# Optimization experiments

Measured on AMD Instinct MI355X. Metric: run time of the kernel, lower is better.

The kernel has to match this reference:

```python
import jax, jax.numpy as jnp
import numpy as np

B, N, M, C = 2, 8192, 8192, 3
SRC_W = 1.0  # src_weight * loss_src_weight
DST_W = 1.0  # dst_weight * loss_dst_weight


def setup_inputs() -> dict:
    key = jax.random.key(0)
    k1, k2 = jax.random.split(key)
    source = jax.random.normal(k1, (B, N, C), dtype=jnp.float32)
    target = jax.random.normal(k2, (B, M, C), dtype=jnp.float32)
    return {"source": source, "target": target}


def reference(source, target):
    # mode='l2' -> mse_loss(none) summed over C = squared euclidean distance
    # distance: [B, N, M]
    diff = source[:, :, None, :] - target[:, None, :, :]  # [B,N,M,C]
    distance = jnp.sum(diff * diff, axis=-1)
    src2dst = jnp.min(distance, axis=2)       # [B,N]
    indices1 = jnp.argmin(distance, axis=2)   # [B,N]
    dst2src = jnp.min(distance, axis=1)       # [B,M]
    indices2 = jnp.argmin(distance, axis=1)   # [B,M]
    # reduction='mean', weights all 1.0
    loss_src = jnp.mean(src2dst * SRC_W)
    loss_dst = jnp.mean(dst2src * DST_W)
    return (loss_src, loss_dst, indices1, indices2)
```

## Files before the change

### kernel.cpp

```cpp
#include <hip/hip_runtime.h>
#include <math.h>


static constexpr int Bn = 2;
static constexpr int Nn = 8192;
static constexpr int THR = 256;
static constexpr int QPL = 4;
static constexpr int RT = 1024;
static constexpr int WROWS = 256;
static constexpr int CT = 64;
static constexpr int TB = 8;
static constexpr int CB = 4096;

typedef __attribute__((ext_vector_type(2))) float f32x2;

__device__ __forceinline__ f32x2 pk_add(f32x2 a, f32x2 b) {
    f32x2 r;
    asm("v_pk_add_f32 %0, %1, %2" : "=v"(r) : "v"(a), "v"(b));
    return r;
}
__device__ __forceinline__ f32x2 pk_mul(f32x2 a, f32x2 b) {
    f32x2 r;
    asm("v_pk_mul_f32 %0, %1, %2" : "=v"(r) : "v"(a), "v"(b));
    return r;
}
__device__ __forceinline__ f32x2 fmin2(f32x2 a, f32x2 b) {
    f32x2 r;
    r.x = fminf(a.x, b.x);
    r.y = fminf(a.y, b.y);
    return r;
}
__device__ __forceinline__ f32x2 dist3x2(f32x2 tx, f32x2 ty, f32x2 tz,
                                         f32x2 nqx, f32x2 nqy, f32x2 nqz) {
    f32x2 dx = pk_add(tx, nqx);
    f32x2 dy = pk_add(ty, nqy);
    f32x2 dz = pk_add(tz, nqz);
    f32x2 px = pk_mul(dx, dx);
    f32x2 py = pk_mul(dy, dy);
    f32x2 pz = pk_mul(dz, dz);
    return pk_add(pk_add(px, py), pz);
}

template <int PAT>
__device__ __forceinline__ float swzx(float x) {
    return __int_as_float(__builtin_amdgcn_ds_swizzle(__float_as_int(x), PAT));
}
static constexpr int SWZ_X1  = 0x041F;
static constexpr int SWZ_X2  = 0x081F;
static constexpr int SWZ_X4  = 0x101F;
static constexpr int SWZ_X8  = 0x201F;
static constexpr int SWZ_X16 = 0x401F;

__device__ __forceinline__ float dist3(float s0, float s1, float s2,
                                       float q0, float q1, float q2) {
    #pragma clang fp contract(off)
    float d0 = s0 - q0;
    float d1 = s1 - q1;
    float d2 = s2 - q2;
    return (d0 * d0 + d1 * d1) + d2 * d2;
}

__global__ void cd_init(unsigned long long* __restrict__ ws) {
    int i = blockIdx.x * blockDim.x + threadIdx.x;
    if (i < 2 * Bn * Nn) ws[i] = 0xFFFFFFFFFFFFFFFFULL;
}

__global__ __launch_bounds__(THR, 4) void cd_tile(const float* __restrict__ S,
                                                  const float* __restrict__ T,
                                                  unsigned long long* __restrict__ ws) {
    const int b = blockIdx.z;
    const int rbase = blockIdx.x * RT;
    const int cbase = blockIdx.y * CT;
    unsigned long long* wsRow = ws + (size_t)b * Nn;
    unsigned long long* wsCol = ws + 2 * Nn + (size_t)b * Nn;

    __shared__ alignas(16) float lt[3][CT];
    __shared__ unsigned long long lwcol[4][CT];
    if (threadIdx.x < CT * 3 / 4) {
        float4 v4 = ((const float4*)(T + ((size_t)b * Nn + cbase) * 3))[threadIdx.x];
        int e = threadIdx.x * 4;
        lt[(e    ) % 3][(e    ) / 3] = v4.x;
        lt[(e + 1) % 3][(e + 1) / 3] = v4.y;
        lt[(e + 2) % 3][(e + 2) / 3] = v4.z;
        lt[(e + 3) % 3][(e + 3) / 3] = v4.w;
    }
    __syncthreads();

    const int w = threadIdx.x >> 6;
    const int L = threadIdx.x & 63;
    const int rowA = rbase + w * WROWS + L;
    const unsigned int anchor = (unsigned int)(rbase + w * WROWS);

    f32x2 nqx[QPL], nqy[QPL], nqz[QPL];
    #pragma unroll
    for (int k = 0; k < QPL; ++k) {
        const float* p = S + ((size_t)b * Nn + rowA + k * 64) * 3;
        float a0 = -p[0], a1 = -p[1], a2 = -p[2];
        nqx[k].x = a0; nqx[k].y = a0;
        nqy[k].x = a1; nqy[k].y = a1;
        nqz[k].x = a2; nqz[k].y = a2;
    }

    float best[QPL];
    int bb[QPL];
    #pragma unroll
    for (int k = 0; k < QPL; ++k) { best[k] = INFINITY; bb[k] = 0; }

    #pragma unroll 2
    for (int jb = 0; jb < CT / TB; ++jb) {
        const f32x2* lx = (const f32x2*)&lt[0][jb * TB];
        const f32x2* ly = (const f32x2*)&lt[1][jb * TB];
        const f32x2* lz = (const f32x2*)&lt[2][jb * TB];
        f32x2 tx[4], ty[4], tz[4];
        #pragma unroll
        for (int p = 0; p < 4; ++p) { tx[p] = lx[p]; ty[p] = ly[p]; tz[p] = lz[p]; }

        f32x2 cm2[4];
        #pragma unroll
        for (int k = 0; k < QPL; ++k) {
            f32x2 dd[4];
            #pragma unroll
            for (int p = 0; p < 4; ++p)
                dd[p] = dist3x2(tx[p], ty[p], tz[p], nqx[k], nqy[k], nqz[k]);
            #pragma unroll
            for (int p = 0; p < 4; ++p)
                cm2[p] = (k == 0) ? dd[p] : fmin2(cm2[p], dd[p]);
            float m0 = fminf(fminf(dd[0].x, dd[0].y), dd[1].x);
            float m1 = fminf(fminf(dd[1].y, dd[2].x), dd[2].y);
            float m2 = fminf(dd[3].x, dd[3].y);
            float bmin = fminf(fminf(m0, m1), m2);
            if (bmin < best[k]) { best[k] = bmin; bb[k] = cbase + jb * TB; }
        }

        float cmf0 = cm2[0].x, cmf1 = cm2[0].y, cmf2 = cm2[1].x, cmf3 = cm2[1].y;
        float cmf4 = cm2[2].x, cmf5 = cm2[2].y, cmf6 = cm2[3].x, cmf7 = cm2[3].y;

        const bool u1 = (L & 1);
        float a0 = fminf(u1 ? cmf4 : cmf0, swzx<SWZ_X1>(u1 ? cmf0 : cmf4));
        float a1 = fminf(u1 ? cmf5 : cmf1, swzx<SWZ_X1>(u1 ? cmf1 : cmf5));
        float a2 = fminf(u1 ? cmf6 : cmf2, swzx<SWZ_X1>(u1 ? cmf2 : cmf6));
        float a3 = fminf(u1 ? cmf7 : cmf3, swzx<SWZ_X1>(u1 ? cmf3 : cmf7));
        const bool u2 = (L & 2);
        float b0 = fminf(u2 ? a2 : a0, swzx<SWZ_X2>(u2 ? a0 : a2));
        float b1 = fminf(u2 ? a3 : a1, swzx<SWZ_X2>(u2 ? a1 : a3));
        const bool u4 = (L & 4);
        float c0 = fminf(u4 ? b1 : b0, swzx<SWZ_X4>(u4 ? b0 : b1));
        c0 = fminf(c0, swzx<SWZ_X8>(c0));
        c0 = fminf(c0, swzx<SWZ_X16>(c0));
        c0 = fminf(c0, __shfl_xor(c0, 32, 64));

        if (L < TB) {
            const int c = 4 * (L & 1) + 2 * ((L >> 1) & 1) + ((L >> 2) & 1);
            unsigned long long pk =
                ((unsigned long long)__float_as_uint(c0) << 32) | anchor;
            lwcol[w][jb * TB + c] = pk;
        }
    }

    #pragma unroll
    for (int k = 0; k < QPL; ++k) {
        unsigned long long pk =
            ((unsigned long long)__float_as_uint(best[k]) << 32) |
            (unsigned int)bb[k];
        atomicMin(&wsRow[rowA + k * 64], pk);
    }

    __syncthreads();
    if (threadIdx.x < CT) {
        unsigned long long x0 = lwcol[0][threadIdx.x];
        unsigned long long x1 = lwcol[1][threadIdx.x];
        unsigned long long x2 = lwcol[2][threadIdx.x];
        unsigned long long x3 = lwcol[3][threadIdx.x];
        unsigned long long m01 = x0 < x1 ? x0 : x1;
        unsigned long long m23 = x2 < x3 ? x2 : x3;
        unsigned long long m = m01 < m23 ? m01 : m23;
        atomicMin(&wsCol[cbase + threadIdx.x], m);
    }
}

__global__ __launch_bounds__(256) void cd_fin(const unsigned long long* __restrict__ ws,
                                              const float* __restrict__ S,
                                              const float* __restrict__ T,
                                              float* __restrict__ out,
                                              float* __restrict__ pr,
                                              float* __restrict__ pc) {
    __shared__ float red[4];
    const int tid = threadIdx.x;

    if (blockIdx.x < CB) {
        const int e = blockIdx.x * 4 + (tid >> 6);
        const int L = tid & 63;
        const int b = e >> 13;
        const int col = e & 8191;

        unsigned long long p = ws[2 * Nn + e];
        const float m = __uint_as_float((unsigned int)(p >> 32));
        const int A = (int)(unsigned int)(p & 0xFFFFFFFFu);

        const float* tc = T + ((size_t)b * Nn + col) * 3;
        const float t0 = tc[0], t1 = tc[1], t2 = tc[2];

        const float4* Sp = (const float4*)(S + ((size_t)b * Nn + A + L * 4) * 3);
        const float4 x0 = Sp[0], x1 = Sp[1], x2 = Sp[2];

        int found = 0x7FFFFFFF;
        if (dist3(x2.y, x2.z, x2.w, t0, t1, t2) == m) found = A + L * 4 + 3;
        if (dist3(x1.z, x1.w, x2.x, t0, t1, t2) == m) found = A + L * 4 + 2;
        if (dist3(x0.w, x1.x, x1.y, t0, t1, t2) == m) found = A + L * 4 + 1;
        if (dist3(x0.x, x0.y, x0.z, t0, t1, t2) == m) found = A + L * 4 + 0;
        #pragma unroll
        for (int mask = 1; mask < 64; mask <<= 1)
            found = min(found, __shfl_xor(found, mask, 64));
        if (L == 0) out[2 + 2 * Nn + e] = (float)found;

        if (L == 0) red[tid >> 6] = m;
        __syncthreads();
        if (tid == 0) pc[blockIdx.x] = (red[0] + red[1]) + (red[2] + red[3]);
    } else {
        const int j = (blockIdx.x - CB) * 256 + tid;
        const int b = j >> 13;
        const int row = j & 8191;

        unsigned long long p = ws[j];
        const float dist = __uint_as_float((unsigned int)(p >> 32));
        const int cb = (int)(unsigned int)(p & 0xFFFFFFFFu);

        const float* Pp = S + ((size_t)b * Nn + row) * 3;
        const float s0 = Pp[0], s1 = Pp[1], s2 = Pp[2];
        const float4* Qb = (const float4*)(T + ((size_t)b * Nn + cb) * 3);
        const float4 y0 = Qb[0], y1 = Qb[1], y2 = Qb[2];
        const float4 y3 = Qb[3], y4 = Qb[4], y5 = Qb[5];

        int idx = cb;
        if (dist3(s0, s1, s2, y5.y, y5.z, y5.w) == dist) idx = cb + 7;
        if (dist3(s0, s1, s2, y4.z, y4.w, y5.x) == dist) idx = cb + 6;
        if (dist3(s0, s1, s2, y3.w, y4.x, y4.y) == dist) idx = cb + 5;
        if (dist3(s0, s1, s2, y3.x, y3.y, y3.z) == dist) idx = cb + 4;
        if (dist3(s0, s1, s2, y2.y, y2.z, y2.w) == dist) idx = cb + 3;
        if (dist3(s0, s1, s2, y1.z, y1.w, y2.x) == dist) idx = cb + 2;
        if (dist3(s0, s1, s2, y0.w, y1.x, y1.y) == dist) idx = cb + 1;
        if (dist3(s0, s1, s2, y0.x, y0.y, y0.z) == dist) idx = cb + 0;
        out[2 + j] = (float)idx;

        float sum = dist;
        for (int off = 32; off > 0; off >>= 1) sum += __shfl_down(sum, off, 64);
        if ((tid & 63) == 0) red[tid >> 6] = sum;
        __syncthreads();
        if (tid == 0)
            pr[blockIdx.x - CB] = (red[0] + red[1]) + (red[2] + red[3]);
    }
}

__global__ __launch_bounds__(256) void cd_combine(const float* __restrict__ pr,
                                                  const float* __restrict__ pc,
                                                  float* __restrict__ out) {
    const int tid = threadIdx.x;
    float s1 = (tid < 64) ? pr[tid] : 0.0f;
    float s2 = 0.0f;
    for (int i = tid; i < CB; i += 256) s2 += pc[i];

    __shared__ float r1[4], r2[4];
    for (int off = 32; off > 0; off >>= 1) {
        s1 += __shfl_down(s1, off, 64);
        s2 += __shfl_down(s2, off, 64);
    }
    if ((tid & 63) == 0) { r1[tid >> 6] = s1; r2[tid >> 6] = s2; }
    __syncthreads();
    if (tid == 0) {
        out[0] = ((r1[0] + r1[1]) + (r1[2] + r1[3])) / (float)(Bn * Nn);
        out[1] = ((r2[0] + r2[1]) + (r2[2] + r2[3])) / (float)(Bn * Nn);
    }
}

static constexpr int FPTS = 256;
static constexpr int FCHUNK = 1024;

__global__ void cd_zero2(float* __restrict__ out) { out[0] = 0.0f; out[1] = 0.0f; }

__global__ __launch_bounds__(FPTS) void cd_dir_direct(const float* __restrict__ P,
                                                      const float* __restrict__ Q,
                                                      int nP, int nQ,
                                                      float* __restrict__ idx_out,
                                                      float* __restrict__ loss_out,
                                                      float inv_count) {
    __shared__ float lq[FCHUNK * 3];
    __shared__ float red[FPTS / 64];
    const int b = blockIdx.z;
    const int i = blockIdx.x * FPTS + threadIdx.x;
    const float* Pp = P + ((size_t)b * nP + i) * 3;
    const float s0 = Pp[0], s1 = Pp[1], s2 = Pp[2];

    float best = INFINITY;
    int bi = 0;
    for (int c = 0; c < nQ / FCHUNK; ++c) {
        __syncthreads();
        const float* Qb = Q + ((size_t)b * nQ + (size_t)c * FCHUNK) * 3;
        for (int j = threadIdx.x; j < FCHUNK * 3; j += FPTS) lq[j] = Qb[j];
        __syncthreads();
        #pragma unroll 4
        for (int m = 0; m < FCHUNK; ++m) {
            float dist = dist3(s0, s1, s2, lq[3 * m], lq[3 * m + 1], lq[3 * m + 2]);
            if (dist < best) { best = dist; bi = c * FCHUNK + m; }
        }
    }
    idx_out[(size_t)b * nP + i] = (float)bi;

    float v = best;
    for (int off = 32; off > 0; off >>= 1) v += __shfl_down(v, off, 64);
    const int wid = threadIdx.x >> 6;
    if ((threadIdx.x & 63) == 0) red[wid] = v;
    __syncthreads();
    if (threadIdx.x == 0) {
        float a = 0.0f;
        for (int w = 0; w < FPTS / 64; ++w) a += red[w];
        atomicAdd(loss_out, a * inv_count);
    }
}

extern "C" void kernel_launch(void* const* d_in, const int* in_sizes, int n_in,
                              void* d_out, int out_size, void* d_ws, size_t ws_size,
                              hipStream_t stream) {
    const float* src = (const float*)d_in[0];
    const float* tgt = (const float*)d_in[1];
    float* out = (float*)d_out;
    const int TOTAL = 2 * Bn * Nn;
    const size_t need = (size_t)TOTAL * sizeof(unsigned long long)
                      + (64 + CB) * sizeof(float);

    if (ws_size >= need) {
        unsigned long long* ws = (unsigned long long*)d_ws;
        float* pr = (float*)(ws + TOTAL);
        float* pc = pr + 64;
        cd_init<<<(TOTAL + 255) / 256, 256, 0, stream>>>(ws);
        cd_tile<<<dim3(Nn / RT, Nn / CT, Bn), THR, 0, stream>>>(src, tgt, ws);
        cd_fin<<<CB + 64, 256, 0, stream>>>(ws, src, tgt, out, pr, pc);
        cd_combine<<<1, 256, 0, stream>>>(pr, pc, out);
    } else {
        cd_zero2<<<1, 1, 0, stream>>>(out);
        cd_dir_direct<<<dim3(Nn / FPTS, 1, Bn), FPTS, 0, stream>>>(
            src, tgt, Nn, Nn, out + 2, out + 0, 1.0f / (float)(Bn * Nn));
        cd_dir_direct<<<dim3(Nn / FPTS, 1, Bn), FPTS, 0, stream>>>(
            tgt, src, Nn, Nn, out + 2 + Bn * Nn, out + 1, 1.0f / (float)(Bn * Nn));
    }
}
```

Baseline: 54.59 us.

## Replace global 64-bit atomicMin with per-tile partial buffers reduced in finalize

Each tile block now writes its packed (distance, index) row and column minima to its own slot in per-tile partial arrays instead of calling atomicMin on a shared workspace. The finalize kernel then min-reduces across all 128 column tiles for each row and all 8 row tiles for each column. This drops the init kernel and removes atomic contention. In exchange it needs about 17 MB of workspace and adds a serial 128-load reduction per row in only 64 finalize blocks. If the workspace is too small, execution falls back to the slow direct path.

```diff
diff --git a/kernel.cpp b/kernel.cpp
--- a/kernel.cpp
+++ b/kernel.cpp
@@ -11,6 +11,9 @@
 static constexpr int CT = 64;
 static constexpr int TB = 8;
 static constexpr int CB = 4096;
+static constexpr int NRB = Nn / RT;
+static constexpr int NCB = Nn / CT;
+static constexpr int ENT = Bn * Nn;
 
 typedef __attribute__((ext_vector_type(2))) float f32x2;
 
@@ -60,19 +63,15 @@
     return (d0 * d0 + d1 * d1) + d2 * d2;
 }
 
-__global__ void cd_init(unsigned long long* __restrict__ ws) {
-    int i = blockIdx.x * blockDim.x + threadIdx.x;
-    if (i < 2 * Bn * Nn) ws[i] = 0xFFFFFFFFFFFFFFFFULL;
-}
-
 __global__ __launch_bounds__(THR, 4) void cd_tile(const float* __restrict__ S,
                                                   const float* __restrict__ T,
-                                                  unsigned long long* __restrict__ ws) {
+                                                  unsigned long long* __restrict__ rowpart,
+                                                  unsigned long long* __restrict__ colpart) {
     const int b = blockIdx.z;
     const int rbase = blockIdx.x * RT;
     const int cbase = blockIdx.y * CT;
-    unsigned long long* wsRow = ws + (size_t)b * Nn;
-    unsigned long long* wsCol = ws + 2 * Nn + (size_t)b * Nn;
+    unsigned long long* rp = rowpart + (size_t)blockIdx.y * ENT + (size_t)b * Nn;
+    unsigned long long* cp = colpart + (size_t)blockIdx.x * ENT + (size_t)b * Nn;
 
     __shared__ alignas(16) float lt[3][CT];
     __shared__ unsigned long long lwcol[4][CT];
@@ -162,7 +161,7 @@
         unsigned long long pk =
             ((unsigned long long)__float_as_uint(best[k]) << 32) |
             (unsigned int)bb[k];
-        atomicMin(&wsRow[rowA + k * 64], pk);
+        rp[rowA + k * 64] = pk;
     }
 
     __syncthreads();
@@ -174,11 +173,12 @@
         unsigned long long m01 = x0 < x1 ? x0 : x1;
         unsigned long long m23 = x2 < x3 ? x2 : x3;
         unsigned long long m = m01 < m23 ? m01 : m23;
-        atomicMin(&wsCol[cbase + threadIdx.x], m);
-    }
-}
-
-__global__ __launch_bounds__(256) void cd_fin(const unsigned long long* __restrict__ ws,
+        cp[cbase + threadIdx.x] = m;
+    }
+}
+
+__global__ __launch_bounds__(256) void cd_fin(const unsigned long long* __restrict__ rowpart,
+                                              const unsigned long long* __restrict__ colpart,
                                               const float* __restrict__ S,
                                               const float* __restrict__ T,
                                               float* __restrict__ out,
@@ -193,7 +193,12 @@
         const int b = e >> 13;
         const int col = e & 8191;
 
-        unsigned long long p = ws[2 * Nn + e];
+        unsigned long long p = colpart[e];
+        #pragma unroll
+        for (int rb = 1; rb < NRB; ++rb) {
+            unsigned long long q = colpart[(size_t)rb * ENT + e];
+            p = q < p ? q : p;
+        }
         const float m = __uint_as_float((unsigned int)(p >> 32));
         const int A = (int)(unsigned int)(p & 0xFFFFFFFFu);
 
@@ -221,7 +226,12 @@
         const int b = j >> 13;
         const int row = j & 8191;
 
-        unsigned long long p = ws[j];
+        unsigned long long p = rowpart[j];
+        #pragma unroll 8
+        for (int cb2 = 1; cb2 < NCB; ++cb2) {
+            unsigned long long q = rowpart[(size_t)cb2 * ENT + j];
+            p = q < p ? q : p;
+        }
         const float dist = __uint_as_float((unsigned int)(p >> 32));
         const int cb = (int)(unsigned int)(p & 0xFFFFFFFFu);
 
@@ -323,17 +333,18 @@
     const float* src = (const float*)d_in[0];
     const float* tgt = (const float*)d_in[1];
     float* out = (float*)d_out;
-    const int TOTAL = 2 * Bn * Nn;
-    const size_t need = (size_t)TOTAL * sizeof(unsigned long long)
+    const size_t ROWP = (size_t)NCB * ENT;
+    const size_t COLP = (size_t)NRB * ENT;
+    const size_t need = (ROWP + COLP) * sizeof(unsigned long long)
                       + (64 + CB) * sizeof(float);
 
     if (ws_size >= need) {
-        unsigned long long* ws = (unsigned long long*)d_ws;
-        float* pr = (float*)(ws + TOTAL);
+        unsigned long long* rowpart = (unsigned long long*)d_ws;
+        unsigned long long* colpart = rowpart + ROWP;
+        float* pr = (float*)(colpart + COLP);
         float* pc = pr + 64;
-        cd_init<<<(TOTAL + 255) / 256, 256, 0, stream>>>(ws);
-        cd_tile<<<dim3(Nn / RT, Nn / CT, Bn), THR, 0, stream>>>(src, tgt, ws);
-        cd_fin<<<CB + 64, 256, 0, stream>>>(ws, src, tgt, out, pr, pc);
+        cd_tile<<<dim3(Nn / RT, Nn / CT, Bn), THR, 0, stream>>>(src, tgt, rowpart, colpart);
+        cd_fin<<<CB + 64, 256, 0, stream>>>(rowpart, colpart, src, tgt, out, pr, pc);
         cd_combine<<<1, 256, 0, stream>>>(pr, pc, out);
     } else {
         cd_zero2<<<1, 1, 0, stream>>>(out);
```

Result: slower. 67.97 us (+24.5%).

## Batch column-min reductions across all tiles into one transpose-style butterfly

Applied to the files above, without the earlier changes.

Instead of doing a separate cross-lane min reduction for each of the 8 column blocks (with most lanes idle at the end), the kernel keeps per-block partial minima in registers for all 8 blocks and then runs a single recursive-halving butterfly. Each level both exchanges and halves the data, so all 64 lanes end up holding one distinct column result and write it directly. This cuts the number of swizzle/shuffle operations and the predicated LDS writes. In exchange it raises register pressure from the fully unrolled loop and the 32-float accumulator array, which could hurt occupancy.

```diff
diff --git a/kernel.cpp b/kernel.cpp
--- a/kernel.cpp
+++ b/kernel.cpp
@@ -10,6 +10,7 @@
 static constexpr int WROWS = 256;
 static constexpr int CT = 64;
 static constexpr int TB = 8;
+static constexpr int NJB = CT / TB;
 static constexpr int CB = 4096;
 
 typedef __attribute__((ext_vector_type(2))) float f32x2;
@@ -106,8 +107,10 @@
     #pragma unroll
     for (int k = 0; k < QPL; ++k) { best[k] = INFINITY; bb[k] = 0; }
 
-    #pragma unroll 2
-    for (int jb = 0; jb < CT / TB; ++jb) {
+    f32x2 A[NJB][4];
+
+    #pragma unroll
+    for (int jb = 0; jb < NJB; ++jb) {
         const f32x2* lx = (const f32x2*)&lt[0][jb * TB];
         const f32x2* ly = (const f32x2*)&lt[1][jb * TB];
         const f32x2* lz = (const f32x2*)&lt[2][jb * TB];
@@ -115,7 +118,6 @@
         #pragma unroll
         for (int p = 0; p < 4; ++p) { tx[p] = lx[p]; ty[p] = ly[p]; tz[p] = lz[p]; }
 
-        f32x2 cm2[4];
         #pragma unroll
         for (int k = 0; k < QPL; ++k) {
             f32x2 dd[4];
@@ -124,38 +126,59 @@
                 dd[p] = dist3x2(tx[p], ty[p], tz[p], nqx[k], nqy[k], nqz[k]);
             #pragma unroll
             for (int p = 0; p < 4; ++p)
-                cm2[p] = (k == 0) ? dd[p] : fmin2(cm2[p], dd[p]);
+                A[jb][p] = (k == 0) ? dd[p] : fmin2(A[jb][p], dd[p]);
             float m0 = fminf(fminf(dd[0].x, dd[0].y), dd[1].x);
             float m1 = fminf(fminf(dd[1].y, dd[2].x), dd[2].y);
             float m2 = fminf(dd[3].x, dd[3].y);
             float bmin = fminf(fminf(m0, m1), m2);
             if (bmin < best[k]) { best[k] = bmin; bb[k] = cbase + jb * TB; }
         }
-
-        float cmf0 = cm2[0].x, cmf1 = cm2[0].y, cmf2 = cm2[1].x, cmf3 = cm2[1].y;
-        float cmf4 = cm2[2].x, cmf5 = cm2[2].y, cmf6 = cm2[3].x, cmf7 = cm2[3].y;
-
-        const bool u1 = (L & 1);
-        float a0 = fminf(u1 ? cmf4 : cmf0, swzx<SWZ_X1>(u1 ? cmf0 : cmf4));
-        float a1 = fminf(u1 ? cmf5 : cmf1, swzx<SWZ_X1>(u1 ? cmf1 : cmf5));
-        float a2 = fminf(u1 ? cmf6 : cmf2, swzx<SWZ_X1>(u1 ? cmf2 : cmf6));
-        float a3 = fminf(u1 ? cmf7 : cmf3, swzx<SWZ_X1>(u1 ? cmf3 : cmf7));
-        const bool u2 = (L & 2);
-        float b0 = fminf(u2 ? a2 : a0, swzx<SWZ_X2>(u2 ? a0 : a2));
-        float b1 = fminf(u2 ? a3 : a1, swzx<SWZ_X2>(u2 ? a1 : a3));
-        const bool u4 = (L & 4);
-        float c0 = fminf(u4 ? b1 : b0, swzx<SWZ_X4>(u4 ? b0 : b1));
-        c0 = fminf(c0, swzx<SWZ_X8>(c0));
-        c0 = fminf(c0, swzx<SWZ_X16>(c0));
-        c0 = fminf(c0, __shfl_xor(c0, 32, 64));
-
-        if (L < TB) {
-            const int c = 4 * (L & 1) + 2 * ((L >> 1) & 1) + ((L >> 2) & 1);
-            unsigned long long pk =
-                ((unsigned long long)__float_as_uint(c0) << 32) | anchor;
-            lwcol[w][jb * TB + c] = pk;
+    }
+
+    const bool l0 = L & 1, l1 = L & 2, l2 = L & 4, l3 = L & 8, l4 = L & 16;
+    float n0[NJB][4];
+    #pragma unroll
+    for (int j = 0; j < NJB; ++j)
+        #pragma unroll
+        for (int p = 0; p < 4; ++p) {
+            float keep = l0 ? A[j][p].y : A[j][p].x;
+            float send = l0 ? A[j][p].x : A[j][p].y;
+            n0[j][p] = fminf(keep, swzx<SWZ_X1>(send));
         }
-    }
+    float n1[NJB][2];
+    #pragma unroll
+    for (int j = 0; j < NJB; ++j)
+        #pragma unroll
+        for (int p = 0; p < 2; ++p) {
+            float keep = l1 ? n0[j][2 * p + 1] : n0[j][2 * p];
+            float send = l1 ? n0[j][2 * p] : n0[j][2 * p + 1];
+            n1[j][p] = fminf(keep, swzx<SWZ_X2>(send));
+        }
+    float n2[NJB];
+    #pragma unroll
+    for (int j = 0; j < NJB; ++j) {
+        float keep = l2 ? n1[j][1] : n1[j][0];
+        float send = l2 ? n1[j][0] : n1[j][1];
+        n2[j] = fminf(keep, swzx<SWZ_X4>(send));
+    }
+    float n3[4];
+    #pragma unroll
+    for (int j = 0; j < 4; ++j) {
+        float keep = l3 ? n2[2 * j + 1] : n2[2 * j];
+        float send = l3 ? n2[2 * j] : n2[2 * j + 1];
+        n3[j] = fminf(keep, swzx<SWZ_X8>(send));
+    }
+    float n4[2];
+    #pragma unroll
+    for (int j = 0; j < 2; ++j) {
+        float keep = l4 ? n3[2 * j + 1] : n3[2 * j];
+        float send = l4 ? n3[2 * j] : n3[2 * j + 1];
+        n4[j] = fminf(keep, swzx<SWZ_X16>(send));
+    }
+    float keep5 = (L & 32) ? n4[1] : n4[0];
+    float send5 = (L & 32) ? n4[0] : n4[1];
+    float r = fminf(keep5, __shfl_xor(send5, 32, 64));
+    lwcol[w][L] = ((unsigned long long)__float_as_uint(r) << 32) | anchor;
 
     #pragma unroll
     for (int k = 0; k < QPL; ++k) {
```

Result: faster. 53.49 us (-2.0%).
